# Kernel optimization log

Measured on AMD Instinct MI355X. Metric: run time of the kernel, lower is better.

Reference implementation:

```python
import jax, jax.numpy as jnp
import numpy as np

N_HEAD = 8
NORM_GROUPS = 32
EPS = 1e-6


def setup_inputs() -> dict:
    key = jax.random.key(0)
    ks = jax.random.split(key, 9)
    B, C, H, W, D = 1, 256, 16, 16, 16
    COND = 512
    x = jax.random.normal(ks[0], (B, C, H, W, D), dtype=jnp.float32)
    cond = jax.random.normal(ks[1], (B, COND), dtype=jnp.float32)
    # AdaGN linear scale/shift (torch Linear: weight [C, cond_dim], bias [C])
    w_scale = jax.random.normal(ks[2], (C, COND), dtype=jnp.float32) * 0.02
    b_scale = jax.random.normal(ks[3], (C,), dtype=jnp.float32) * 0.02
    w_shift = jax.random.normal(ks[4], (C, COND), dtype=jnp.float32) * 0.02
    b_shift = jax.random.normal(ks[5], (C,), dtype=jnp.float32) * 0.02
    # 1x1x1 conv3d weights collapse to matrices: qkv [3C, C] (no bias), out [C, C] + bias
    w_qkv = jax.random.normal(ks[6], (3 * C, C), dtype=jnp.float32) * (1.0 / np.sqrt(C))
    w_out = jax.random.normal(ks[7], (C, C), dtype=jnp.float32) * (1.0 / np.sqrt(C))
    b_out = jax.random.normal(ks[8], (C,), dtype=jnp.float32) * 0.02
    return {"x": x, "cond": cond, "w_scale": w_scale, "b_scale": b_scale,
            "w_shift": w_shift, "b_shift": b_shift, "w_qkv": w_qkv,
            "w_out": w_out, "b_out": b_out}


def _ada_gn(x, cond, w_scale, b_scale, w_shift, b_shift):
    B, C, H, W, D = x.shape
    G = NORM_GROUPS
    xg = x.reshape(B, G, C // G, H, W, D)
    mean = jnp.mean(xg, axis=(2, 3, 4, 5), keepdims=True)
    var = jnp.var(xg, axis=(2, 3, 4, 5), keepdims=True)
    x_norm = ((xg - mean) * jax.lax.rsqrt(var + EPS)).reshape(B, C, H, W, D)
    scale = (cond @ w_scale.T + b_scale)[:, :, None, None, None]  # [B,C,1,1,1]
    shift = (cond @ w_shift.T + b_shift)[:, :, None, None, None]
    return x_norm * (1.0 + scale) + shift


def reference(x, cond, w_scale, b_scale, w_shift, b_shift, w_qkv, w_out, b_out):
    B, C, H, W, D = x.shape
    nh = N_HEAD
    hd = C // nh
    N = H * W * D  # flattened spatial tokens
    norm = _ada_gn(x, cond, w_scale, b_scale, w_shift, b_shift)
    # 1x1x1 conv == channel matmul
    qkv = jnp.einsum('oc,bchwd->bohwd', w_qkv, norm)        # [B,3C,H,W,D]
    qkv = qkv.reshape(B, nh, 3 * hd, N)
    q, k, v = jnp.split(qkv, 3, axis=2)                      # each [B,nh,hd,N]
    attn = jnp.einsum('bnci,bncj->bnij', q, k) / jnp.sqrt(jnp.float32(C))
    attn = jax.nn.softmax(attn, axis=-1)                     # [B,nh,N,N]
    out = jnp.einsum('bnij,bncj->bnci', attn, v)             # [B,nh,hd,N]
    out = out.reshape(B, C, H, W, D)
    out = jnp.einsum('oc,bchwd->bohwd', w_out, out) + b_out[None, :, None, None, None]
    return out + x
```

## Files before the change

kernel.cpp:

```cpp
#include <hip/hip_runtime.h>
#include <math.h>

#define CCH 256
#define NN  4096
#define NHEAD 8
#define CONDD 512

typedef __attribute__((ext_vector_type(8))) short short8;
typedef __attribute__((ext_vector_type(4))) float f32x4;
typedef __attribute__((ext_vector_type(16))) float f32x16;

static __device__ __forceinline__ short f2bf(float f) {
    union { float f; uint32_t u; } v; v.f = f;
    uint32_t r = v.u + 0x7fffu + ((v.u >> 16) & 1u);
    return (short)(r >> 16);
}

static __device__ __forceinline__ uint32_t cvt_pk_bf16(float a, float b) {
    uint32_t r;
    asm("v_cvt_pk_bf16_f32 %0, %1, %2" : "=v"(r) : "v"(a), "v"(b));
    return r;
}

__global__ __launch_bounds__(256) void front_fused(const float* __restrict__ x,
                                                   const float* __restrict__ cond,
                                                   const float* __restrict__ w_scale,
                                                   const float* __restrict__ b_scale,
                                                   const float* __restrict__ w_shift,
                                                   const float* __restrict__ b_shift,
                                                   const float* __restrict__ wq,
                                                   const float* __restrict__ wo,
                                                   float* __restrict__ partial,
                                                   float* __restrict__ scale,
                                                   float* __restrict__ shift,
                                                   short* __restrict__ wqb,
                                                   short* __restrict__ wob) {
    __shared__ float rs[4], rss[4];
    int bb = blockIdx.x;
    int t = threadIdx.x;
    if (bb < 256) {
        const float4* p = (const float4*)(x + bb * 4096);
        float s = 0.f, ss = 0.f;
        for (int k = t; k < 1024; k += 256) {
            float4 v = p[k];
            s += v.x + v.y + v.z + v.w;
            ss += v.x * v.x + v.y * v.y + v.z * v.z + v.w * v.w;
        }
        #pragma unroll
        for (int off = 32; off; off >>= 1) { s += __shfl_xor(s, off); ss += __shfl_xor(ss, off); }
        int wid = t >> 6;
        if ((t & 63) == 0) { rs[wid] = s; rss[wid] = ss; }
        __syncthreads();
        if (t == 0) {
            partial[2 * bb] = rs[0] + rs[1] + rs[2] + rs[3];
            partial[2 * bb + 1] = rss[0] + rss[1] + rss[2] + rss[3];
        }
    } else if (bb < 512) {
        int idx4 = (bb - 256) * 256 + t;
        if (idx4 < 49152) {
            float4 v = ((const float4*)wq)[idx4];
            uint2 u;
            u.x = cvt_pk_bf16(v.x, v.y);
            u.y = cvt_pk_bf16(v.z, v.w);
            *(uint2*)&wqb[idx4 * 4] = u;
        } else {
            float4 v = ((const float4*)wo)[idx4 - 49152];
            uint2 u;
            u.x = cvt_pk_bf16(v.x, v.y);
            u.y = cvt_pk_bf16(v.z, v.w);
            *(uint2*)&wob[(idx4 - 49152) * 4] = u;
        }
    } else {
        int o = (bb - 512) * 4 + (t >> 6);
        int lane = t & 63;
        float ds = 0.f, dh = 0.f;
        for (int k = lane; k < CONDD; k += 64) {
            float cv = cond[k];
            ds += cv * w_scale[o * CONDD + k];
            dh += cv * w_shift[o * CONDD + k];
        }
        #pragma unroll
        for (int off = 32; off; off >>= 1) { ds += __shfl_xor(ds, off); dh += __shfl_xor(dh, off); }
        if (lane == 0) { scale[o] = ds + b_scale[o]; shift[o] = dh + b_shift[o]; }
    }
}

__global__ __launch_bounds__(256, 4) void qkv_fused(const float* __restrict__ x,
                                                    const float* __restrict__ partial,
                                                    const float* __restrict__ scale,
                                                    const float* __restrict__ shift,
                                                    const short* __restrict__ wqb,
                                                    short* __restrict__ qtb, short* __restrict__ ktb,
                                                    short* __restrict__ vcb) {
    __shared__ float Af[256], Bf[256];
    __shared__ __align__(16) short nt[16384];

    int t = threadIdx.x;
    int o0 = blockIdx.x * 128;
    int i0 = blockIdx.y * 64;

    {
        int c = t;
        int g = c >> 3;
        float s = 0.f, ss = 0.f;
        #pragma unroll
        for (int ch = 0; ch < 8; ++ch) {
            s += partial[(g * 8 + ch) * 2];
            ss += partial[(g * 8 + ch) * 2 + 1];
        }
        float mean = s * (1.0f / 32768.0f);
        float var = ss * (1.0f / 32768.0f) - mean * mean;
        float rstd = rsqrtf(var + 1e-6f);
        float a = rstd * (1.0f + scale[c]);
        Af[c] = a;
        Bf[c] = shift[c] - mean * a;
    }
    __syncthreads();

    #pragma unroll
    for (int e = 0; e < 8; ++e) {
        int task = e * 256 + t;
        int il = task & 63;
        int slot = task >> 6;
        int c0 = slot * 8;
        union { short s[8]; short8 v; } pk;
        #pragma unroll
        for (int j = 0; j < 8; ++j) {
            float v = x[(c0 + j) * NN + i0 + il];
            pk.s[j] = f2bf(v * Af[c0 + j] + Bf[c0 + j]);
        }
        *(short8*)((char*)nt + slot * 1024 + il * 16) = pk.v;
    }
    __syncthreads();

    int w = t >> 6, lane = t & 63, li = lane & 15, lg = lane >> 4;
    int irow = w * 16 + li;

    f32x4 acc[8] = {{0,0,0,0},{0,0,0,0},{0,0,0,0},{0,0,0,0},
                    {0,0,0,0},{0,0,0,0},{0,0,0,0},{0,0,0,0}};
    const short* abase = wqb + (o0 + li) * 256 + 8 * lg;
    #pragma unroll
    for (int ks = 0; ks < 8; ++ks) {
        int slot = ks * 4 + lg;
        short8 bfrag = *(const short8*)((char*)nt + slot * 1024 + irow * 16);
        #pragma unroll
        for (int f = 0; f < 8; ++f) {
            short8 afrag = *(const short8*)(abase + f * 16 * 256 + ks * 32);
            acc[f] = __builtin_amdgcn_mfma_f32_16x16x32_bf16(afrag, bfrag, acc[f], 0, 0, 0);
        }
    }
    int i = i0 + irow;
    #pragma unroll
    for (int f = 0; f < 8; ++f) {
        #pragma unroll
        for (int r = 0; r < 4; ++r) {
            int o = o0 + 16 * f + 4 * lg + r;
            float v = acc[f][r];
            int h = o / 96;
            int rr = o - h * 96;
            int cc = rr & 31;
            int kind = rr >> 5;
            if (kind == 0)      qtb[(h * NN + i) * 32 + cc] = f2bf(v * (0.0625f * 1.44269504f));
            else if (kind == 1) ktb[(h * NN + i) * 32 + cc] = f2bf(v);
            else                vcb[(h * 32 + cc) * NN + i] = f2bf(v);
        }
    }
}

__global__ __launch_bounds__(512, 4) void attention_mfma(const short* __restrict__ qtb,
                                                         const short* __restrict__ ktb,
                                                         const short* __restrict__ vcb,
                                                         float* __restrict__ pacc,
                                                         float* __restrict__ plsum) {
    __shared__ __align__(16) char lds[49152];

    int bid = blockIdx.x;
    int h = bid & 7;
    int qb = (bid >> 3) & 15;
    int kh = bid >> 7;
    int t = threadIdx.x;
    int w = t >> 6, lane = t & 63, l31 = lane & 31, hi = lane >> 5;

    int qbase = qb * 256 + w * 32;
    const short* qrow = qtb + (h * NN + qbase + l31) * 32;
    short8 qf0 = *(const short8*)(qrow + 8 * hi);
    short8 qf1 = *(const short8*)(qrow + 16 + 8 * hi);
    asm volatile("s_waitcnt vmcnt(0)" ::: "memory");

    const char* src0;
    const char* src1;
    int ldsoff0, ldsoff1, step;
    if (w < 4) {
        int row_l = lane >> 2, g_lds = lane & 3;
        int g_glob = g_lds ^ (row_l & 3);
        const char* kbase = (const char*)ktb + (size_t)(h * NN + kh * 1024) * 64;
        int s0 = 2 * w, s1 = 2 * w + 1;
        src0 = kbase + ((s0 >> 2) * 64 + (s0 & 3) * 16 + row_l) * 64 + g_glob * 16;
        src1 = kbase + ((s1 >> 2) * 64 + (s1 & 3) * 16 + row_l) * 64 + g_glob * 16;
        ldsoff0 = s0 * 1024;
        ldsoff1 = s1 * 1024;
        step = 8192;
    } else {
        int row_l = lane >> 3, vs_lds = lane & 7;
        int vg = vs_lds ^ row_l;
        const char* vbase = (const char*)vcb + (size_t)(h * 32) * (NN * 2) + kh * 2048;
        int s0 = 2 * (w - 4), s1 = 2 * (w - 4) + 1;
        src0 = vbase + (size_t)((s0 & 3) * 8 + row_l) * (NN * 2) + (s0 >> 2) * 128 + vg * 16;
        src1 = vbase + (size_t)((s1 & 3) * 8 + row_l) * (NN * 2) + (s1 >> 2) * 128 + vg * 16;
        ldsoff0 = 8192 + s0 * 1024;
        ldsoff1 = 8192 + s1 * 1024;
        step = 256;
    }

    f32x16 acc = {0,0,0,0,0,0,0,0,0,0,0,0,0,0,0,0};
    const f32x16 zero16 = {0,0,0,0,0,0,0,0,0,0,0,0,0,0,0,0};
    float lsum = 0.f;

    #define ISSUE(st, b) do { \
        __builtin_amdgcn_global_load_lds((const uint32_t*)(src0 + (st) * step), \
            (uint32_t*)(lds + (b) * 16384 + ldsoff0), 16, 0, 0); \
        __builtin_amdgcn_global_load_lds((const uint32_t*)(src1 + (st) * step), \
            (uint32_t*)(lds + (b) * 16384 + ldsoff1), 16, 0, 0); \
    } while (0)

    #define COMPUTE(b) do { \
        const char* bb_ = lds + (b) * 16384; \
        _Pragma("unroll") \
        for (int chunk = 0; chunk < 2; ++chunk) { \
            _Pragma("unroll") \
            for (int half = 0; half < 2; ++half) { \
                int jl = half * 32; \
                int R = jl + l31; \
                int rx = R & 3; \
                const char* kr = bb_ + chunk * 4096 + R * 64; \
                short8 kf0 = *(const short8*)(kr + (((hi) ^ rx) << 4)); \
                short8 kf1 = *(const short8*)(kr + (((2 + hi) ^ rx) << 4)); \
                const char* vr = bb_ + 8192 + chunk * 4096 + l31 * 128; \
                int cx = l31 & 7; \
                int sv = (jl >> 3) + hi; \
                short8 vf0 = *(const short8*)(vr + ((sv ^ cx) << 4)); \
                short8 vf1 = *(const short8*)(vr + (((sv + 2) ^ cx) << 4)); \
                __builtin_amdgcn_s_setprio(1); \
                f32x16 s = __builtin_amdgcn_mfma_f32_32x32x16_bf16(kf0, qf0, zero16, 0, 0, 0); \
                s = __builtin_amdgcn_mfma_f32_32x32x16_bf16(kf1, qf1, s, 0, 0, 0); \
                __builtin_amdgcn_s_setprio(0); \
                float p[16]; \
                _Pragma("unroll") \
                for (int r = 0; r < 16; ++r) p[r] = __builtin_amdgcn_exp2f(s[r]); \
                float u0 = 0.f, u1 = 0.f; \
                _Pragma("unroll") \
                for (int r = 0; r < 4; ++r) { u0 += p[r] + p[4 + r]; u1 += p[8 + r] + p[12 + r]; } \
                lsum += u0 + u1; \
                auto A1 = __builtin_amdgcn_permlane32_swap(cvt_pk_bf16(p[0], p[1]),   cvt_pk_bf16(p[4], p[5]),   false, false); \
                auto A2 = __builtin_amdgcn_permlane32_swap(cvt_pk_bf16(p[2], p[3]),   cvt_pk_bf16(p[6], p[7]),   false, false); \
                auto A3 = __builtin_amdgcn_permlane32_swap(cvt_pk_bf16(p[8], p[9]),   cvt_pk_bf16(p[12], p[13]), false, false); \
                auto A4 = __builtin_amdgcn_permlane32_swap(cvt_pk_bf16(p[10], p[11]), cvt_pk_bf16(p[14], p[15]), false, false); \
                union PF { uint32_t u[4]; short8 s8; }; \
                PF f1, f2; \
                f1.u[0] = A1[0]; f1.u[1] = A2[0]; f1.u[2] = A1[1]; f1.u[3] = A2[1]; \
                f2.u[0] = A3[0]; f2.u[1] = A4[0]; f2.u[2] = A3[1]; f2.u[3] = A4[1]; \
                __builtin_amdgcn_s_setprio(1); \
                acc = __builtin_amdgcn_mfma_f32_32x32x16_bf16(vf0, f1.s8, acc, 0, 0, 0); \
                acc = __builtin_amdgcn_mfma_f32_32x32x16_bf16(vf1, f2.s8, acc, 0, 0, 0); \
                __builtin_amdgcn_s_setprio(0); \
            } \
        } \
    } while (0)

    ISSUE(0, 0);
    ISSUE(1, 1);
    ISSUE(2, 2);
    asm volatile("s_waitcnt vmcnt(4)" ::: "memory");
    __builtin_amdgcn_s_barrier();

    #pragma unroll
    for (int st = 0; st < 5; ++st) {
        COMPUTE(st % 3);
        __builtin_amdgcn_s_barrier();
        ISSUE(st + 3, st % 3);
        asm volatile("s_waitcnt vmcnt(4)" ::: "memory");
        __builtin_amdgcn_s_barrier();
    }
    COMPUTE(2);
    __builtin_amdgcn_s_barrier();
    asm volatile("s_waitcnt vmcnt(2)" ::: "memory");
    __builtin_amdgcn_s_barrier();
    COMPUTE(0);
    __builtin_amdgcn_s_barrier();
    asm volatile("s_waitcnt vmcnt(0)" ::: "memory");
    __builtin_amdgcn_s_barrier();
    COMPUTE(1);

    #undef ISSUE
    #undef COMPUTE

    lsum += __shfl_xor(lsum, 32);

    int qg = qbase + l31;
    float* pb = pacc + (size_t)((kh * 8 + h) * 32) * NN + qg;
    #pragma unroll
    for (int r = 0; r < 16; ++r) {
        int c = (r & 3) + 8 * (r >> 2) + 4 * hi;
        pb[c * NN] = acc[r];
    }
    if (hi == 0) plsum[(size_t)(kh * 8 + h) * NN + qg] = lsum;
}

__global__ __launch_bounds__(256) void attn_merge(const float* __restrict__ pacc,
                                                  const float* __restrict__ plsum,
                                                  short* __restrict__ attnT) {
    __shared__ float tile[64][33];
    __shared__ float invl[64];
    int it = blockIdx.x;
    int h = blockIdx.y;
    int t = threadIdx.x;
    int i0 = it * 64;
    int c = t >> 3, ic = (t & 7) * 8;
    const float* p0 = pacc + (size_t)(h * 32 + c) * NN + i0 + ic;
    #pragma unroll
    for (int k = 0; k < 8; ++k) {
        float s = 0.f;
        #pragma unroll
        for (int q4 = 0; q4 < 4; ++q4) s += p0[(size_t)q4 * 8 * 32 * NN + k];
        tile[ic + k][c] = s;
    }
    if (t < 64) {
        float ls = 0.f;
        #pragma unroll
        for (int q4 = 0; q4 < 4; ++q4) ls += plsum[(size_t)(q4 * 8 + h) * NN + i0 + t];
        invl[t] = 1.0f / ls;
    }
    __syncthreads();
    int i = t >> 2, cs = (t & 3) * 8;
    float iv = invl[i];
    const float* tr = &tile[i][cs];
    uint4 o;
    o.x = cvt_pk_bf16(tr[0] * iv, tr[1] * iv);
    o.y = cvt_pk_bf16(tr[2] * iv, tr[3] * iv);
    o.z = cvt_pk_bf16(tr[4] * iv, tr[5] * iv);
    o.w = cvt_pk_bf16(tr[6] * iv, tr[7] * iv);
    *(uint4*)&attnT[(i0 + i) * 256 + h * 32 + cs] = o;
}

__global__ __launch_bounds__(256) void proj_gemm(const short* __restrict__ wob,
                                                 const short* __restrict__ attnT,
                                                 const float* __restrict__ b_out,
                                                 const float* __restrict__ x,
                                                 float* __restrict__ out) {
    int t = threadIdx.x;
    int w = t >> 6, lane = t & 63, li = lane & 15, lg = lane >> 4;
    int o0 = blockIdx.x * 32;
    int i0 = blockIdx.y * 64 + w * 16;
    f32x4 acc[2] = {{0,0,0,0},{0,0,0,0}};
    const short* bbase = attnT + (i0 + li) * 256 + 8 * lg;
    const short* abase = wob + (o0 + li) * 256 + 8 * lg;
    #pragma unroll
    for (int ks = 0; ks < 8; ++ks) {
        short8 bfrag = *(const short8*)(bbase + ks * 32);
        #pragma unroll
        for (int f = 0; f < 2; ++f) {
            short8 afrag = *(const short8*)(abase + f * 16 * 256 + ks * 32);
            acc[f] = __builtin_amdgcn_mfma_f32_16x16x32_bf16(afrag, bfrag, acc[f], 0, 0, 0);
        }
    }
    int i = i0 + li;
    #pragma unroll
    for (int f = 0; f < 2; ++f) {
        #pragma unroll
        for (int r = 0; r < 4; ++r) {
            int o = o0 + 16 * f + 4 * lg + r;
            out[o * NN + i] = acc[f][r] + b_out[o] + x[o * NN + i];
        }
    }
}

extern "C" void kernel_launch(void* const* d_in, const int* in_sizes, int n_in,
                              void* d_out, int out_size, void* d_ws, size_t ws_size,
                              hipStream_t stream) {
    const float* x       = (const float*)d_in[0];
    const float* cond    = (const float*)d_in[1];
    const float* w_scale = (const float*)d_in[2];
    const float* b_scale = (const float*)d_in[3];
    const float* w_shift = (const float*)d_in[4];
    const float* b_shift = (const float*)d_in[5];
    const float* w_qkv   = (const float*)d_in[6];
    const float* w_out   = (const float*)d_in[7];
    const float* b_out   = (const float*)d_in[8];
    float* out = (float*)d_out;

    float* ws = (float*)d_ws;
    float* scale   = ws;
    float* shift   = ws + 256;
    float* partial = ws + 512;
    short* qtb = (short*)(ws + 1024);
    short* ktb = qtb + 1048576;
    short* vcb = ktb + 1048576;
    short* attnT = vcb + 1048576;
    short* wqb = attnT + 1048576;
    short* wob = wqb + 196608;
    float* pacc  = (float*)(wob + 65536);
    float* plsum = pacc + (size_t)4 * 8 * 32 * NN;

    front_fused<<<576, 256, 0, stream>>>(x, cond, w_scale, b_scale, w_shift, b_shift,
                                         w_qkv, w_out, partial, scale, shift, wqb, wob);
    qkv_fused<<<dim3(6, 64), 256, 0, stream>>>(x, partial, scale, shift, wqb, qtb, ktb, vcb);
    attention_mfma<<<512, 512, 0, stream>>>(qtb, ktb, vcb, pacc, plsum);
    attn_merge<<<dim3(64, 8), 256, 0, stream>>>(pacc, plsum, attnT);
    proj_gemm<<<dim3(8, 64), 256, 0, stream>>>(wob, attnT, b_out, x, out);
}
```

Measured before the change: 72.05 us.

## Process two query tiles per wave and split keys eight ways in attention

```diff
diff --git a/kernel.cpp b/kernel.cpp
--- a/kernel.cpp
+++ b/kernel.cpp
@@ -176,15 +176,18 @@
 
     int bid = blockIdx.x;
     int h = bid & 7;
-    int qb = (bid >> 3) & 15;
-    int kh = bid >> 7;
+    int qb = (bid >> 3) & 7;
+    int kh = bid >> 6;
     int t = threadIdx.x;
     int w = t >> 6, lane = t & 63, l31 = lane & 31, hi = lane >> 5;
 
-    int qbase = qb * 256 + w * 32;
-    const short* qrow = qtb + (h * NN + qbase + l31) * 32;
-    short8 qf0 = *(const short8*)(qrow + 8 * hi);
-    short8 qf1 = *(const short8*)(qrow + 16 + 8 * hi);
+    int qbase = qb * 512 + w * 64;
+    const short* qrowA = qtb + (h * NN + qbase + l31) * 32;
+    const short* qrowB = qtb + (h * NN + qbase + 32 + l31) * 32;
+    short8 qfA0 = *(const short8*)(qrowA + 8 * hi);
+    short8 qfA1 = *(const short8*)(qrowA + 16 + 8 * hi);
+    short8 qfB0 = *(const short8*)(qrowB + 8 * hi);
+    short8 qfB1 = *(const short8*)(qrowB + 16 + 8 * hi);
     asm volatile("s_waitcnt vmcnt(0)" ::: "memory");
 
     const char* src0;
@@ -193,7 +196,7 @@
     if (w < 4) {
         int row_l = lane >> 2, g_lds = lane & 3;
         int g_glob = g_lds ^ (row_l & 3);
-        const char* kbase = (const char*)ktb + (size_t)(h * NN + kh * 1024) * 64;
+        const char* kbase = (const char*)ktb + (size_t)(h * NN + kh * 512) * 64;
         int s0 = 2 * w, s1 = 2 * w + 1;
         src0 = kbase + ((s0 >> 2) * 64 + (s0 & 3) * 16 + row_l) * 64 + g_glob * 16;
         src1 = kbase + ((s1 >> 2) * 64 + (s1 & 3) * 16 + row_l) * 64 + g_glob * 16;
@@ -203,7 +206,7 @@
     } else {
         int row_l = lane >> 3, vs_lds = lane & 7;
         int vg = vs_lds ^ row_l;
-        const char* vbase = (const char*)vcb + (size_t)(h * 32) * (NN * 2) + kh * 2048;
+        const char* vbase = (const char*)vcb + (size_t)(h * 32) * (NN * 2) + kh * 1024;
         int s0 = 2 * (w - 4), s1 = 2 * (w - 4) + 1;
         src0 = vbase + (size_t)((s0 & 3) * 8 + row_l) * (NN * 2) + (s0 >> 2) * 128 + vg * 16;
         src1 = vbase + (size_t)((s1 & 3) * 8 + row_l) * (NN * 2) + (s1 >> 2) * 128 + vg * 16;
@@ -212,15 +215,42 @@
         step = 256;
     }
 
-    f32x16 acc = {0,0,0,0,0,0,0,0,0,0,0,0,0,0,0,0};
+    f32x16 accA = {0,0,0,0,0,0,0,0,0,0,0,0,0,0,0,0};
+    f32x16 accB = {0,0,0,0,0,0,0,0,0,0,0,0,0,0,0,0};
     const f32x16 zero16 = {0,0,0,0,0,0,0,0,0,0,0,0,0,0,0,0};
-    float lsum = 0.f;
+    float lsumA = 0.f, lsumB = 0.f;
 
     #define ISSUE(st, b) do { \
         __builtin_amdgcn_global_load_lds((const uint32_t*)(src0 + (st) * step), \
             (uint32_t*)(lds + (b) * 16384 + ldsoff0), 16, 0, 0); \
         __builtin_amdgcn_global_load_lds((const uint32_t*)(src1 + (st) * step), \
             (uint32_t*)(lds + (b) * 16384 + ldsoff1), 16, 0, 0); \
+    } while (0)
+
+    #define TILE(q0, q1, vv0, vv1, kk0, kk1, ACC, LSUM) do { \
+        __builtin_amdgcn_s_setprio(1); \
+        f32x16 s = __builtin_amdgcn_mfma_f32_32x32x16_bf16(kk0, q0, zero16, 0, 0, 0); \
+        s = __builtin_amdgcn_mfma_f32_32x32x16_bf16(kk1, q1, s, 0, 0, 0); \
+        __builtin_amdgcn_s_setprio(0); \
+        float p[16]; \
+        _Pragma("unroll") \
+        for (int r = 0; r < 16; ++r) p[r] = __builtin_amdgcn_exp2f(s[r]); \
+        float u0 = 0.f, u1 = 0.f; \
+        _Pragma("unroll") \
+        for (int r = 0; r < 4; ++r) { u0 += p[r] + p[4 + r]; u1 += p[8 + r] + p[12 + r]; } \
+        LSUM += u0 + u1; \
+        auto A1 = __builtin_amdgcn_permlane32_swap(cvt_pk_bf16(p[0], p[1]),   cvt_pk_bf16(p[4], p[5]),   false, false); \
+        auto A2 = __builtin_amdgcn_permlane32_swap(cvt_pk_bf16(p[2], p[3]),   cvt_pk_bf16(p[6], p[7]),   false, false); \
+        auto A3 = __builtin_amdgcn_permlane32_swap(cvt_pk_bf16(p[8], p[9]),   cvt_pk_bf16(p[12], p[13]), false, false); \
+        auto A4 = __builtin_amdgcn_permlane32_swap(cvt_pk_bf16(p[10], p[11]), cvt_pk_bf16(p[14], p[15]), false, false); \
+        union PF { uint32_t u[4]; short8 s8; }; \
+        PF f1, f2; \
+        f1.u[0] = A1[0]; f1.u[1] = A2[0]; f1.u[2] = A1[1]; f1.u[3] = A2[1]; \
+        f2.u[0] = A3[0]; f2.u[1] = A4[0]; f2.u[2] = A3[1]; f2.u[3] = A4[1]; \
+        __builtin_amdgcn_s_setprio(1); \
+        ACC = __builtin_amdgcn_mfma_f32_32x32x16_bf16(vv0, f1.s8, ACC, 0, 0, 0); \
+        ACC = __builtin_amdgcn_mfma_f32_32x32x16_bf16(vv1, f2.s8, ACC, 0, 0, 0); \
+        __builtin_amdgcn_s_setprio(0); \
     } while (0)
 
     #define COMPUTE(b) do { \
@@ -240,29 +270,8 @@
                 int sv = (jl >> 3) + hi; \
                 short8 vf0 = *(const short8*)(vr + ((sv ^ cx) << 4)); \
                 short8 vf1 = *(const short8*)(vr + (((sv + 2) ^ cx) << 4)); \
-                __builtin_amdgcn_s_setprio(1); \
-                f32x16 s = __builtin_amdgcn_mfma_f32_32x32x16_bf16(kf0, qf0, zero16, 0, 0, 0); \
-                s = __builtin_amdgcn_mfma_f32_32x32x16_bf16(kf1, qf1, s, 0, 0, 0); \
-                __builtin_amdgcn_s_setprio(0); \
-                float p[16]; \
-                _Pragma("unroll") \
-                for (int r = 0; r < 16; ++r) p[r] = __builtin_amdgcn_exp2f(s[r]); \
-                float u0 = 0.f, u1 = 0.f; \
-                _Pragma("unroll") \
-                for (int r = 0; r < 4; ++r) { u0 += p[r] + p[4 + r]; u1 += p[8 + r] + p[12 + r]; } \
-                lsum += u0 + u1; \
-                auto A1 = __builtin_amdgcn_permlane32_swap(cvt_pk_bf16(p[0], p[1]),   cvt_pk_bf16(p[4], p[5]),   false, false); \
-                auto A2 = __builtin_amdgcn_permlane32_swap(cvt_pk_bf16(p[2], p[3]),   cvt_pk_bf16(p[6], p[7]),   false, false); \
-                auto A3 = __builtin_amdgcn_permlane32_swap(cvt_pk_bf16(p[8], p[9]),   cvt_pk_bf16(p[12], p[13]), false, false); \
-                auto A4 = __builtin_amdgcn_permlane32_swap(cvt_pk_bf16(p[10], p[11]), cvt_pk_bf16(p[14], p[15]), false, false); \
-                union PF { uint32_t u[4]; short8 s8; }; \
-                PF f1, f2; \
-                f1.u[0] = A1[0]; f1.u[1] = A2[0]; f1.u[2] = A1[1]; f1.u[3] = A2[1]; \
-                f2.u[0] = A3[0]; f2.u[1] = A4[0]; f2.u[2] = A3[1]; f2.u[3] = A4[1]; \
-                __builtin_amdgcn_s_setprio(1); \
-                acc = __builtin_amdgcn_mfma_f32_32x32x16_bf16(vf0, f1.s8, acc, 0, 0, 0); \
-                acc = __builtin_amdgcn_mfma_f32_32x32x16_bf16(vf1, f2.s8, acc, 0, 0, 0); \
-                __builtin_amdgcn_s_setprio(0); \
+                TILE(qfA0, qfA1, vf0, vf1, kf0, kf1, accA, lsumA); \
+                TILE(qfB0, qfB1, vf0, vf1, kf0, kf1, accB, lsumB); \
             } \
         } \
     } while (0)
@@ -273,37 +282,42 @@
     asm volatile("s_waitcnt vmcnt(4)" ::: "memory");
     __builtin_amdgcn_s_barrier();
 
-    #pragma unroll
-    for (int st = 0; st < 5; ++st) {
-        COMPUTE(st % 3);
-        __builtin_amdgcn_s_barrier();
-        ISSUE(st + 3, st % 3);
-        asm volatile("s_waitcnt vmcnt(4)" ::: "memory");
-        __builtin_amdgcn_s_barrier();
-    }
+    COMPUTE(0);
+    __builtin_amdgcn_s_barrier();
+    ISSUE(3, 0);
+    asm volatile("s_waitcnt vmcnt(4)" ::: "memory");
+    __builtin_amdgcn_s_barrier();
+    COMPUTE(1);
+    __builtin_amdgcn_s_barrier();
+    asm volatile("s_waitcnt vmcnt(2)" ::: "memory");
+    __builtin_amdgcn_s_barrier();
     COMPUTE(2);
     __builtin_amdgcn_s_barrier();
-    asm volatile("s_waitcnt vmcnt(2)" ::: "memory");
+    asm volatile("s_waitcnt vmcnt(0)" ::: "memory");
     __builtin_amdgcn_s_barrier();
     COMPUTE(0);
-    __builtin_amdgcn_s_barrier();
-    asm volatile("s_waitcnt vmcnt(0)" ::: "memory");
-    __builtin_amdgcn_s_barrier();
-    COMPUTE(1);
 
     #undef ISSUE
+    #undef TILE
     #undef COMPUTE
 
-    lsum += __shfl_xor(lsum, 32);
-
-    int qg = qbase + l31;
-    float* pb = pacc + (size_t)((kh * 8 + h) * 32) * NN + qg;
+    lsumA += __shfl_xor(lsumA, 32);
+    lsumB += __shfl_xor(lsumB, 32);
+
+    int qgA = qbase + l31;
+    int qgB = qbase + 32 + l31;
+    float* pbA = pacc + (size_t)((kh * 8 + h) * 32) * NN + qgA;
+    float* pbB = pacc + (size_t)((kh * 8 + h) * 32) * NN + qgB;
     #pragma unroll
     for (int r = 0; r < 16; ++r) {
         int c = (r & 3) + 8 * (r >> 2) + 4 * hi;
-        pb[c * NN] = acc[r];
-    }
-    if (hi == 0) plsum[(size_t)(kh * 8 + h) * NN + qg] = lsum;
+        pbA[c * NN] = accA[r];
+        pbB[c * NN] = accB[r];
+    }
+    if (hi == 0) {
+        plsum[(size_t)(kh * 8 + h) * NN + qgA] = lsumA;
+        plsum[(size_t)(kh * 8 + h) * NN + qgB] = lsumB;
+    }
 }
 
 __global__ __launch_bounds__(256) void attn_merge(const float* __restrict__ pacc,
@@ -321,13 +335,13 @@
     for (int k = 0; k < 8; ++k) {
         float s = 0.f;
         #pragma unroll
-        for (int q4 = 0; q4 < 4; ++q4) s += p0[(size_t)q4 * 8 * 32 * NN + k];
+        for (int q8 = 0; q8 < 8; ++q8) s += p0[(size_t)q8 * 8 * 32 * NN + k];
         tile[ic + k][c] = s;
     }
     if (t < 64) {
         float ls = 0.f;
         #pragma unroll
-        for (int q4 = 0; q4 < 4; ++q4) ls += plsum[(size_t)(q4 * 8 + h) * NN + i0 + t];
+        for (int q8 = 0; q8 < 8; ++q8) ls += plsum[(size_t)(q8 * 8 + h) * NN + i0 + t];
         invl[t] = 1.0f / ls;
     }
     __syncthreads();
@@ -399,7 +413,7 @@
     short* wqb = attnT + 1048576;
     short* wob = wqb + 196608;
     float* pacc  = (float*)(wob + 65536);
-    float* plsum = pacc + (size_t)4 * 8 * 32 * NN;
+    float* plsum = pacc + (size_t)8 * 8 * 32 * NN;
 
     front_fused<<<576, 256, 0, stream>>>(x, cond, w_scale, b_scale, w_shift, b_shift,
                                          w_qkv, w_out, partial, scale, shift, wqb, wob);
```

New measurement: 74.77 us. +3.8%, slower.
